# Optimization experiments

Measured on AMD Instinct MI355X. Metric: run time of the kernel, lower is better.

## Reference

```python
import jax, jax.numpy as jnp
import numpy as np

N_HEADS = 6

def setup_inputs() -> dict:
    key = jax.random.key(0)
    k1, k2, k3 = jax.random.split(key, 3)
    B, T, C = 256, 256, 192
    x = jax.random.normal(k1, (B, T, C), dtype=jnp.float32)
    w_qkv = jax.random.normal(k2, (3 * C, C), dtype=jnp.float32) * (1.0 / np.sqrt(C))
    w_out = jax.random.normal(k3, (C, C), dtype=jnp.float32) * (1.0 / np.sqrt(C))
    return {"x": x, "w_qkv": w_qkv, "w_out": w_out}

def reference(x, w_qkv, w_out):
    B, T, C = x.shape
    H = N_HEADS
    D = C // H  # head_dim = 32
    qkv = (x @ w_qkv.T).reshape(B, T, 3, H, D)
    q, k, v = qkv[:, :, 0], qkv[:, :, 1], qkv[:, :, 2]  # [B,T,H,D]
    scale = 1.0 / jnp.sqrt(jnp.asarray(D, dtype=x.dtype))
    scores = jnp.einsum('bqhd,bkhd->bhqk', q, k) * scale  # [B,H,T,T]
    causal = jnp.tril(jnp.ones((T, T), dtype=bool))
    scores = jnp.where(causal[None, None], scores, jnp.finfo(x.dtype).min)
    attn = jax.nn.softmax(scores, axis=-1)
    y = jnp.einsum('bhqk,bkhd->bqhd', attn, v).reshape(B, T, C)
    return y @ w_out.T
```

## Files before the change

### kernel.cpp

```cpp
#include <hip/hip_runtime.h>


using f32x4  = __attribute__((ext_vector_type(4))) float;
using bf16x8 = __attribute__((ext_vector_type(8))) __bf16;
using u16x8  = __attribute__((ext_vector_type(8))) unsigned short;
using i32x4  = __attribute__((ext_vector_type(4))) int;

constexpr int Bn = 256;
constexpr int Tn = 256;
constexpr int Cn = 192;
constexpr int Hn = 6;
constexpr int Dn = 32;
constexpr int Mn = Bn * Tn;
constexpr float QSCALE = 0.2550533f;

__device__ __forceinline__ unsigned short f2bf(float f) {
  unsigned int u = __builtin_bit_cast(unsigned int, f);
  u += 0x7fffu + ((u >> 16) & 1u);
  return (unsigned short)(u >> 16);
}

__device__ __forceinline__ unsigned int cvtpk(float lo, float hi) {
  unsigned int r;
  asm("v_cvt_pk_bf16_f32 %0, %1, %2" : "=v"(r) : "v"(lo), "v"(hi));
  return r;
}

__device__ __forceinline__ u16x8 pack8(float4 a, float4 b, float s) {
  uint4 w;
  w.x = cvtpk(a.x * s, a.y * s);
  w.y = cvtpk(a.z * s, a.w * s);
  w.z = cvtpk(b.x * s, b.y * s);
  w.w = cvtpk(b.z * s, b.w * s);
  return __builtin_bit_cast(u16x8, w);
}

__device__ __forceinline__ f32x4 mfma16x16x32(u16x8 a, u16x8 b, f32x4 c) {
  return __builtin_amdgcn_mfma_f32_16x16x32_bf16(
      __builtin_bit_cast(bf16x8, a), __builtin_bit_cast(bf16x8, b), c, 0, 0, 0);
}

__global__ __launch_bounds__(256, 2) void k_qkv(const float* __restrict__ x,
                                                const float* __restrict__ wqkv,
                                                unsigned short* __restrict__ qg,
                                                unsigned short* __restrict__ kg,
                                                unsigned short* __restrict__ vg) {
  __shared__ u16x8 Bsf[2][1536];
  const int tid = threadIdx.x;
  const int m0 = blockIdx.x * 128;
  const int w = tid >> 6, lane = tid & 63, llo = lane & 15, lhi = lane >> 4;

  u16x8 af[6][2];
#pragma unroll
  for (int i = 0; i < 2; ++i) {
    const float* xr = x + (size_t)(m0 + 32 * w + 16 * i + llo) * Cn + lhi * 8;
#pragma unroll
    for (int ks = 0; ks < 6; ++ks) {
      float4 a0 = *reinterpret_cast<const float4*>(xr + ks * 32);
      float4 a1 = *reinterpret_cast<const float4*>(xr + ks * 32 + 4);
      af[ks][i] = pack8(a0, a1, 1.0f);
    }
  }

  {
    const int n0 = 0;
#pragma unroll
    for (int it = 0; it < 6; ++it) {
      int p = tid + it * 256;
      int j = p / 384, rem = p - j * 384;
      int ks = rem >> 6, l2 = rem & 63;
      int row = j * 16 + (l2 & 15), col = ks * 32 + ((l2 >> 4) << 3);
      const float* wp = wqkv + (size_t)(n0 + row) * Cn + col;
      float4 a0 = *reinterpret_cast<const float4*>(wp);
      float4 a1 = *reinterpret_cast<const float4*>(wp + 4);
      Bsf[0][p] = pack8(a0, a1, QSCALE);
    }
  }
  __syncthreads();

  for (int nt = 0; nt < 9; ++nt) {
    const int cur = nt & 1;
    float4 wr[6][2];
    if (nt < 8) {
      const int n0 = (nt + 1) * 64;
#pragma unroll
      for (int it = 0; it < 6; ++it) {
        int p = tid + it * 256;
        int j = p / 384, rem = p - j * 384;
        int ks = rem >> 6, l2 = rem & 63;
        int row = j * 16 + (l2 & 15), col = ks * 32 + ((l2 >> 4) << 3);
        const float* wp = wqkv + (size_t)(n0 + row) * Cn + col;
        wr[it][0] = *reinterpret_cast<const float4*>(wp);
        wr[it][1] = *reinterpret_cast<const float4*>(wp + 4);
      }
    }
    f32x4 acc[2][4] = {};
#pragma unroll
    for (int j = 0; j < 4; ++j) {
      u16x8 bb[6];
#pragma unroll
      for (int ks = 0; ks < 6; ++ks)
        bb[ks] = Bsf[cur][(j * 6 + ks) * 64 + lane];
#pragma unroll
      for (int ks = 0; ks < 6; ++ks)
#pragma unroll
        for (int i = 0; i < 2; ++i)
          acc[i][j] = mfma16x16x32(af[ks][i], bb[ks], acc[i][j]);
    }
    if (nt < 8) {
      const float sc = (nt + 1 < 3) ? QSCALE : 1.0f;
#pragma unroll
      for (int it = 0; it < 6; ++it) {
        int p = tid + it * 256;
        Bsf[cur ^ 1][p] = pack8(wr[it][0], wr[it][1], sc);
      }
    }
    const int sidx = nt / 3;
    unsigned short* dst = (sidx == 0) ? qg : (sidx == 1) ? kg : vg;
    const int nbase = (nt - sidx * 3) * 64;
#pragma unroll
    for (int i = 0; i < 2; ++i)
#pragma unroll
      for (int j = 0; j < 4; ++j)
#pragma unroll
        for (int r = 0; r < 4; ++r) {
          int mg = m0 + 32 * w + 16 * i + lhi * 4 + r;
          int nn = nbase + 16 * j + llo;
          int h = nn >> 5, d = nn & 31;
          int bb_ = mg >> 8, t = mg & 255;
          dst[(size_t)(bb_ * Hn + h) * (Tn * Dn) + t * Dn + d] = f2bf(acc[i][j][r]);
        }
    if (nt < 8) __syncthreads();
  }
}

__global__ __launch_bounds__(256, 3) void k_attn(const unsigned short* __restrict__ qg,
                                                 const unsigned short* __restrict__ kg,
                                                 const unsigned short* __restrict__ vg,
                                                 unsigned short* __restrict__ yg) {
  __shared__ unsigned short Ks[256][40];
  __shared__ unsigned short Vt[32][264];
  const int bh = blockIdx.x;
  const int b = bh / Hn, h = bh - b * Hn;
  const size_t base = (size_t)bh * Tn * Dn;
  const int tid = threadIdx.x;

  {
    int row = tid;
    const unsigned short* kp = kg + base + (size_t)row * Dn;
    *reinterpret_cast<uint4*>(&Ks[row][0])  = *reinterpret_cast<const uint4*>(kp + 0);
    *reinterpret_cast<uint4*>(&Ks[row][8])  = *reinterpret_cast<const uint4*>(kp + 8);
    *reinterpret_cast<uint4*>(&Ks[row][16]) = *reinterpret_cast<const uint4*>(kp + 16);
    *reinterpret_cast<uint4*>(&Ks[row][24]) = *reinterpret_cast<const uint4*>(kp + 24);
    const unsigned short* vp = vg + base + (size_t)row * Dn;
    u16x8 v0 = *reinterpret_cast<const u16x8*>(vp + 0);
    u16x8 v1 = *reinterpret_cast<const u16x8*>(vp + 8);
    u16x8 v2 = *reinterpret_cast<const u16x8*>(vp + 16);
    u16x8 v3 = *reinterpret_cast<const u16x8*>(vp + 24);
#pragma unroll
    for (int e = 0; e < 8; ++e) {
      Vt[e][row]      = v0[e];
      Vt[8 + e][row]  = v1[e];
      Vt[16 + e][row] = v2[e];
      Vt[24 + e][row] = v3[e];
    }
  }
  __syncthreads();

  const int w = tid >> 6, lane = tid & 63, llo = lane & 15, lhi = lane >> 4;
  u16x8 qf[4];
  const unsigned short* qp = qg + base + (size_t)w * 64 * Dn;
#pragma unroll
  for (int i = 0; i < 4; ++i)
    qf[i] = *reinterpret_cast<const u16x8*>(qp + (size_t)(16 * i + llo) * Dn + lhi * 8);

  f32x4 ot[2][4] = {};
  float m_[4], l_[4];
#pragma unroll
  for (int qi = 0; qi < 4; ++qi) { m_[qi] = -1e30f; l_[qi] = 0.f; }

  const int addr0 = (llo + ((lhi & 1) << 5)) << 2;
  const int addr1 = addr0 + 64;

  for (int kt = 0; kt <= w; ++kt) {
    u16x8 kf[4];
#pragma unroll
    for (int kj = 0; kj < 4; ++kj)
      kf[kj] = *reinterpret_cast<const u16x8*>(&Ks[kt * 64 + kj * 16 + llo][lhi * 8]);
    u16x8 vtf[2][2];
#pragma unroll
    for (int ks = 0; ks < 2; ++ks)
#pragma unroll
      for (int dj = 0; dj < 2; ++dj)
        vtf[ks][dj] = *reinterpret_cast<const u16x8*>(&Vt[16 * dj + llo][kt * 64 + ks * 32 + lhi * 8]);

#pragma unroll
    for (int qi = 0; qi < 4; ++qi) {
      f32x4 st[4];
#pragma unroll
      for (int kj = 0; kj < 4; ++kj)
        st[kj] = mfma16x16x32(kf[kj], qf[qi], f32x4{});
      if (kt == w) {
        int ql = 16 * qi + llo;
#pragma unroll
        for (int kj = 0; kj < 4; ++kj)
#pragma unroll
          for (int r = 0; r < 4; ++r) {
            int kl = kj * 16 + lhi * 4 + r;
            st[kj][r] = (kl > ql) ? -1e30f : st[kj][r];
          }
      }
      float x0 = fmaxf(fmaxf(st[0][0], st[0][1]), fmaxf(st[0][2], st[0][3]));
      float x1 = fmaxf(fmaxf(st[1][0], st[1][1]), fmaxf(st[1][2], st[1][3]));
      float x2 = fmaxf(fmaxf(st[2][0], st[2][1]), fmaxf(st[2][2], st[2][3]));
      float x3 = fmaxf(fmaxf(st[3][0], st[3][1]), fmaxf(st[3][2], st[3][3]));
      float mx = fmaxf(fmaxf(x0, x1), fmaxf(x2, x3));
      mx = fmaxf(mx, __shfl_xor(mx, 16));
      mx = fmaxf(mx, __shfl_xor(mx, 32));
      float mn = fmaxf(m_[qi], mx);
      float al = exp2f(m_[qi] - mn);
      float sum = 0.f;
#pragma unroll
      for (int kj = 0; kj < 4; ++kj) {
        float p0 = exp2f(st[kj][0] - mn);
        float p1 = exp2f(st[kj][1] - mn);
        float p2 = exp2f(st[kj][2] - mn);
        float p3 = exp2f(st[kj][3] - mn);
        st[kj][0] = p0; st[kj][1] = p1; st[kj][2] = p2; st[kj][3] = p3;
        sum += (p0 + p1) + (p2 + p3);
      }
      sum += __shfl_xor(sum, 16);
      sum += __shfl_xor(sum, 32);
      l_[qi] = l_[qi] * al + sum;
      m_[qi] = mn;
#pragma unroll
      for (int dj = 0; dj < 2; ++dj)
#pragma unroll
        for (int r = 0; r < 4; ++r)
          ot[dj][qi][r] *= al;

      int pk0[4], pk1[4];
#pragma unroll
      for (int kj = 0; kj < 4; ++kj) {
        pk0[kj] = (int)cvtpk(st[kj][0], st[kj][1]);
        pk1[kj] = (int)cvtpk(st[kj][2], st[kj][3]);
      }
#pragma unroll
      for (int ks = 0; ks < 2; ++ks) {
        i32x4 pw;
#pragma unroll
        for (int j = 0; j < 4; ++j) {
          int addr = (j < 2) ? addr0 : addr1;
          int slo = (j & 1) ? pk1[2 * ks]     : pk0[2 * ks];
          int shi = (j & 1) ? pk1[2 * ks + 1] : pk0[2 * ks + 1];
          int blo = __builtin_amdgcn_ds_bpermute(addr, slo);
          int bhi = __builtin_amdgcn_ds_bpermute(addr, shi);
          pw[j] = (lhi & 2) ? bhi : blo;
        }
        u16x8 pbv = __builtin_bit_cast(u16x8, pw);
#pragma unroll
        for (int dj = 0; dj < 2; ++dj)
          ot[dj][qi] = mfma16x16x32(vtf[ks][dj], pbv, ot[dj][qi]);
      }
    }
  }
#pragma unroll
  for (int qi = 0; qi < 4; ++qi) {
    float rl = 1.0f / l_[qi];
    int t = w * 64 + 16 * qi + llo;
    size_t yo = ((size_t)(b * Tn + t) * Hn + h) * Dn;
#pragma unroll
    for (int dj = 0; dj < 2; ++dj) {
      uint2 pkd;
      pkd.x = cvtpk(ot[dj][qi][0] * rl, ot[dj][qi][1] * rl);
      pkd.y = cvtpk(ot[dj][qi][2] * rl, ot[dj][qi][3] * rl);
      *reinterpret_cast<uint2*>(&yg[yo + 16 * dj + lhi * 4]) = pkd;
    }
  }
}

__global__ __launch_bounds__(256, 2) void k_out(const unsigned short* __restrict__ yg,
                                                const float* __restrict__ wout,
                                                float* __restrict__ out) {
  __shared__ u16x8 Bof[4608];
  const int tid = threadIdx.x;
  const int m0 = blockIdx.x * 128;
  const int w = tid >> 6, lane = tid & 63, llo = lane & 15, lhi = lane >> 4;

#pragma unroll
  for (int it = 0; it < 18; ++it) {
    int p = tid + it * 256;
    int j = p / 384, rem = p - j * 384;
    int ks = rem >> 6, l2 = rem & 63;
    int row = j * 16 + (l2 & 15), col = ks * 32 + ((l2 >> 4) << 3);
    const float* wp = wout + (size_t)row * Cn + col;
    float4 a0 = *reinterpret_cast<const float4*>(wp);
    float4 a1 = *reinterpret_cast<const float4*>(wp + 4);
    Bof[p] = pack8(a0, a1, 1.0f);
  }

  u16x8 af[6][2];
#pragma unroll
  for (int i = 0; i < 2; ++i) {
    const unsigned short* yr = yg + (size_t)(m0 + 32 * w + 16 * i + llo) * Cn + lhi * 8;
#pragma unroll
    for (int ks = 0; ks < 6; ++ks)
      af[ks][i] = *reinterpret_cast<const u16x8*>(yr + ks * 32);
  }
  __syncthreads();

  f32x4 acc[2][12] = {};
#pragma unroll
  for (int j = 0; j < 12; ++j) {
    u16x8 bb[6];
#pragma unroll
    for (int ks = 0; ks < 6; ++ks)
      bb[ks] = Bof[(j * 6 + ks) * 64 + lane];
#pragma unroll
    for (int ks = 0; ks < 6; ++ks)
#pragma unroll
      for (int i = 0; i < 2; ++i)
        acc[i][j] = mfma16x16x32(af[ks][i], bb[ks], acc[i][j]);
  }
#pragma unroll
  for (int i = 0; i < 2; ++i)
#pragma unroll
    for (int j = 0; j < 12; ++j)
#pragma unroll
      for (int r = 0; r < 4; ++r) {
        int mg = m0 + 32 * w + 16 * i + lhi * 4 + r;
        int ng = 16 * j + llo;
        out[(size_t)mg * Cn + ng] = acc[i][j][r];
      }
}

extern "C" void kernel_launch(void* const* d_in, const int* in_sizes, int n_in,
                              void* d_out, int out_size, void* d_ws, size_t ws_size,
                              hipStream_t stream) {
  const float* x    = (const float*)d_in[0];
  const float* wqkv = (const float*)d_in[1];
  const float* wout = (const float*)d_in[2];
  float* out = (float*)d_out;

  const size_t NE = (size_t)Mn * Cn;
  unsigned short* q = (unsigned short*)d_ws;
  unsigned short* k = q + NE;
  unsigned short* v = k + NE;
  unsigned short* y = v + NE;

  k_qkv<<<dim3(Mn / 128), 256, 0, stream>>>(x, wqkv, q, k, v);
  k_attn<<<dim3(Bn * Hn), 256, 0, stream>>>(q, k, v, y);
  k_out<<<dim3(Mn / 128), 256, 0, stream>>>(y, wout, out);
}
```

Before: 105.6 us.

## Split QKV projection across a second grid dimension for Q, K, V sections

The QKV kernel now launches a 2D grid where blockIdx.y selects the Q, K or V section, so each block computes 3 output tiles instead of 9. This triples the block count (512 to 1536) for better CU occupancy and load balance. The cost is that each block reloads and re-converts its x rows three times across the grid. The double-buffered LDS weight tile becomes a single buffer, with register prefetch of the next tile and an added barrier per tile.

```diff
diff --git a/kernel.cpp b/kernel.cpp
--- a/kernel.cpp
+++ b/kernel.cpp
@@ -45,9 +45,10 @@
                                                 unsigned short* __restrict__ qg,
                                                 unsigned short* __restrict__ kg,
                                                 unsigned short* __restrict__ vg) {
-  __shared__ u16x8 Bsf[2][1536];
+  __shared__ u16x8 Bsf[1536];
   const int tid = threadIdx.x;
   const int m0 = blockIdx.x * 128;
+  const int sec = blockIdx.y;
   const int w = tid >> 6, lane = tid & 63, llo = lane & 15, lhi = lane >> 4;
 
   u16x8 af[6][2];
@@ -62,8 +63,9 @@
     }
   }
 
+  float4 wr[6][2];
   {
-    const int n0 = 0;
+    const int n0 = (sec * 3) * 64;
 #pragma unroll
     for (int it = 0; it < 6; ++it) {
       int p = tid + it * 256;
@@ -71,18 +73,21 @@
       int ks = rem >> 6, l2 = rem & 63;
       int row = j * 16 + (l2 & 15), col = ks * 32 + ((l2 >> 4) << 3);
       const float* wp = wqkv + (size_t)(n0 + row) * Cn + col;
-      float4 a0 = *reinterpret_cast<const float4*>(wp);
-      float4 a1 = *reinterpret_cast<const float4*>(wp + 4);
-      Bsf[0][p] = pack8(a0, a1, QSCALE);
-    }
-  }
-  __syncthreads();
-
-  for (int nt = 0; nt < 9; ++nt) {
-    const int cur = nt & 1;
-    float4 wr[6][2];
-    if (nt < 8) {
-      const int n0 = (nt + 1) * 64;
+      wr[it][0] = *reinterpret_cast<const float4*>(wp);
+      wr[it][1] = *reinterpret_cast<const float4*>(wp + 4);
+    }
+  }
+
+  for (int nt = 0; nt < 3; ++nt) {
+    const int gt = sec * 3 + nt;
+    const float sc = (gt < 3) ? QSCALE : 1.0f;
+#pragma unroll
+    for (int it = 0; it < 6; ++it) {
+      int p = tid + it * 256;
+      Bsf[p] = pack8(wr[it][0], wr[it][1], sc);
+    }
+    if (nt < 2) {
+      const int n0 = (gt + 1) * 64;
 #pragma unroll
       for (int it = 0; it < 6; ++it) {
         int p = tid + it * 256;
@@ -94,30 +99,21 @@
         wr[it][1] = *reinterpret_cast<const float4*>(wp + 4);
       }
     }
+    __syncthreads();
+
     f32x4 acc[2][4] = {};
 #pragma unroll
     for (int j = 0; j < 4; ++j) {
       u16x8 bb[6];
 #pragma unroll
       for (int ks = 0; ks < 6; ++ks)
-        bb[ks] = Bsf[cur][(j * 6 + ks) * 64 + lane];
+        bb[ks] = Bsf[(j * 6 + ks) * 64 + lane];
 #pragma unroll
       for (int ks = 0; ks < 6; ++ks)
 #pragma unroll
         for (int i = 0; i < 2; ++i)
           acc[i][j] = mfma16x16x32(af[ks][i], bb[ks], acc[i][j]);
     }
-    if (nt < 8) {
-      const float sc = (nt + 1 < 3) ? QSCALE : 1.0f;
-#pragma unroll
-      for (int it = 0; it < 6; ++it) {
-        int p = tid + it * 256;
-        Bsf[cur ^ 1][p] = pack8(wr[it][0], wr[it][1], sc);
-      }
-    }
-    const int sidx = nt / 3;
-    unsigned short* dst = (sidx == 0) ? qg : (sidx == 1) ? kg : vg;
-    const int nbase = (nt - sidx * 3) * 64;
 #pragma unroll
     for (int i = 0; i < 2; ++i)
 #pragma unroll
@@ -125,12 +121,15 @@
 #pragma unroll
         for (int r = 0; r < 4; ++r) {
           int mg = m0 + 32 * w + 16 * i + lhi * 4 + r;
-          int nn = nbase + 16 * j + llo;
-          int h = nn >> 5, d = nn & 31;
+          int ng = gt * 64 + 16 * j + llo;
+          int s = ng / 192;
+          int rem = ng - s * 192;
+          int h = rem >> 5, d = rem & 31;
           int bb_ = mg >> 8, t = mg & 255;
-          dst[(size_t)(bb_ * Hn + h) * (Tn * Dn) + t * Dn + d] = f2bf(acc[i][j][r]);
+          unsigned short* dst = (s == 0) ? qg : (s == 1) ? kg : vg;
+          dst[((size_t)(bb_ * Hn + h) * Tn + t) * Dn + d] = f2bf(acc[i][j][r]);
         }
-    if (nt < 8) __syncthreads();
+    if (nt < 2) __syncthreads();
   }
 }
 
@@ -292,7 +291,7 @@
     int p = tid + it * 256;
     int j = p / 384, rem = p - j * 384;
     int ks = rem >> 6, l2 = rem & 63;
-    int row = j * 16 + (l2 & 15), col = ks * 32 + ((l2 >> 4) << 3);
+    int row = 16 * j + (l2 & 15), col = ks * 32 + ((l2 >> 4) << 3);
     const float* wp = wout + (size_t)row * Cn + col;
     float4 a0 = *reinterpret_cast<const float4*>(wp);
     float4 a1 = *reinterpret_cast<const float4*>(wp + 4);
@@ -348,7 +347,7 @@
   unsigned short* v = k + NE;
   unsigned short* y = v + NE;
 
-  k_qkv<<<dim3(Mn / 128), 256, 0, stream>>>(x, wqkv, q, k, v);
+  k_qkv<<<dim3(Mn / 128, 3), 256, 0, stream>>>(x, wqkv, q, k, v);
   k_attn<<<dim3(Bn * Hn), 256, 0, stream>>>(q, k, v, y);
   k_out<<<dim3(Mn / 128), 256, 0, stream>>>(y, wout, out);
 }
```

Result: slower. 117.3 us (+11.0%).
